# Optimization experiments

Measured on AMD Instinct MI355X. Metric: run time of the kernel, lower is better.

The kernel has to match this reference:

```python
import jax, jax.numpy as jnp
import numpy as np

T, H, I, E, K = 4096, 2048, 2048, 16, 4
EPS = 1e-6


def setup_inputs() -> dict:
    key = jax.random.key(0)
    ks = jax.random.split(key, 7)
    s = 0.02
    return {
        "x": jax.random.normal(ks[0], (T, H), dtype=jnp.float32),
        "gamma": jnp.ones((H,), dtype=jnp.float32),
        "wg": jax.random.normal(ks[1], (E, H), dtype=jnp.float32) * s,
        "bg": jax.random.normal(ks[2], (E,), dtype=jnp.float32) * s,
        "w1": jax.random.normal(ks[3], (E, I, H), dtype=jnp.float32) * s,  # gate proj
        "w3": jax.random.normal(ks[4], (E, I, H), dtype=jnp.float32) * s,  # up proj
        "w2": jax.random.normal(ks[5], (E, H, I), dtype=jnp.float32) * s,  # down proj
    }


def reference(x, gamma, wg, bg, w1, w3, w2):
    # RMSNorm
    t = x * jax.lax.rsqrt(jnp.mean(x * x, axis=-1, keepdims=True) + EPS) * gamma
    # Router: softmax -> top-k -> renormalize (FusedMoE renormalize=True)
    logits = t @ wg.T + bg                        # [T, E]
    probs = jax.nn.softmax(logits, axis=-1)
    vals, idx = jax.lax.top_k(probs, K)           # [T, K]
    vals = vals / jnp.sum(vals, axis=-1, keepdims=True)
    # Dense [T, E] routing-weight matrix (zeros outside top-k)
    route_w = jnp.einsum("tk,tke->te", vals, jax.nn.one_hot(idx, E, dtype=vals.dtype))
    # Grouped expert GEMMs: scan over experts, accumulate weighted outputs
    def body(acc, p):
        w1e, w3e, w2e, we = p                     # [I,H], [I,H], [H,I], [T]
        h = jax.nn.silu(t @ w1e.T) * (t @ w3e.T)  # [T, I]
        return acc + (h @ w2e.T) * we[:, None], None
    moe_out, _ = jax.lax.scan(body, jnp.zeros_like(x), (w1, w3, w2, route_w.T))
    return x + moe_out
```

## Files before the change

kernel.cpp:

```cpp
#include <hip/hip_runtime.h>
#include <hip/hip_bf16.h>

constexpr int TT = 4096;
constexpr int HH = 2048;
constexpr int II = 2048;
constexpr int EE = 16;
constexpr int KTOP = 4;

typedef __attribute__((ext_vector_type(4))) float f4;
typedef __attribute__((ext_vector_type(8))) short s8;

__device__ __forceinline__ short f2bf(float f) {
    union { __hip_bfloat16 b; short s; } u;
    u.b = __float2bfloat16(f);
    return u.s;
}
__device__ __forceinline__ float bf2f(short s) {
    union { unsigned u; float f; } v;
    v.u = ((unsigned)(unsigned short)s) << 16;
    return v.f;
}

__global__ void k_rmsnorm(const float* __restrict__ x, const float* __restrict__ gamma,
                          short* __restrict__ t16, int* __restrict__ cnt) {
    const int row = blockIdx.x;
    const int tid = threadIdx.x;
    if (row == 0 && tid < EE) cnt[tid] = 0;
    const f4* xr = (const f4*)(x + (size_t)row * HH);
    f4 v0 = xr[tid * 2], v1 = xr[tid * 2 + 1];
    float ss = 0.f;
#pragma unroll
    for (int i = 0; i < 4; i++) { ss += v0[i] * v0[i]; ss += v1[i] * v1[i]; }
#pragma unroll
    for (int m = 32; m >= 1; m >>= 1) ss += __shfl_xor(ss, m);
    __shared__ float red[4];
    const int wid = tid >> 6, lane = tid & 63;
    if (lane == 0) red[wid] = ss;
    __syncthreads();
    const float tot = red[0] + red[1] + red[2] + red[3];
    const float rs = rsqrtf(tot * (1.f / HH) + 1e-6f);
    const f4* gr = (const f4*)gamma;
    f4 g0 = gr[tid * 2], g1 = gr[tid * 2 + 1];
    s8 o;
#pragma unroll
    for (int i = 0; i < 4; i++) {
        o[i]     = f2bf(v0[i] * rs * g0[i]);
        o[4 + i] = f2bf(v1[i] * rs * g1[i]);
    }
    *(s8*)(t16 + (size_t)row * HH + tid * 8) = o;
}

__global__ void k_router(const float* __restrict__ x, const float* __restrict__ gamma,
                         const float* __restrict__ wg, const float* __restrict__ bg,
                         int* __restrict__ cnt, int* __restrict__ lst,
                         float* __restrict__ lwt) {
    const int lane = threadIdx.x & 63;
    const int tok = blockIdx.x * 4 + (threadIdx.x >> 6);
    const float* xr = x + (size_t)tok * HH;
    float t[32];
    float ss = 0.f;
#pragma unroll
    for (int j = 0; j < 32; j++) { float v = xr[lane + 64 * j]; t[j] = v; ss += v * v; }
#pragma unroll
    for (int m = 32; m >= 1; m >>= 1) ss += __shfl_xor(ss, m);
    const float rs = rsqrtf(ss * (1.f / HH) + 1e-6f);
#pragma unroll
    for (int j = 0; j < 32; j++) t[j] *= rs * gamma[lane + 64 * j];

    float logit[EE];
#pragma unroll
    for (int e = 0; e < EE; e++) {
        const float* wrow = wg + (size_t)e * HH;
        float a = 0.f;
#pragma unroll
        for (int j = 0; j < 32; j++) a += t[j] * wrow[lane + 64 * j];
#pragma unroll
        for (int m = 32; m >= 1; m >>= 1) a += __shfl_xor(a, m);
        logit[e] = a + bg[e];
    }
    unsigned chosen = 0u;
    int sel[KTOP]; float sv[KTOP];
#pragma unroll
    for (int k = 0; k < KTOP; k++) {
        float best = -1e30f; int bi = 0;
#pragma unroll
        for (int e = 0; e < EE; e++) {
            bool take = (!((chosen >> e) & 1u)) && (logit[e] > best);
            if (take) { best = logit[e]; bi = e; }
        }
        chosen |= 1u << bi; sel[k] = bi; sv[k] = best;
    }
    const float lmax = sv[0];
    float s = 0.f;
#pragma unroll
    for (int k = 0; k < KTOP; k++) { sv[k] = expf(sv[k] - lmax); s += sv[k]; }
    const float inv = 1.f / s;
    if (lane == 0) {
#pragma unroll
        for (int k = 0; k < KTOP; k++) {
            int e = sel[k];
            int p = atomicAdd(&cnt[e], 1);
            lst[e * TT + p] = tok * KTOP + k;
            lwt[e * TT + p] = sv[k] * inv;
        }
    }
}

__global__ __launch_bounds__(256, 2) void k_gemm_ffn_fused(
        const short* __restrict__ t16, const float* __restrict__ w1,
        const float* __restrict__ w3, short* __restrict__ h,
        const int* __restrict__ cnt, const int* __restrict__ lst) {
    const int e = blockIdx.z;
    const int Me = cnt[e];
    const int m0 = blockIdx.y * 128;
    if (m0 >= Me) return;
    const int n0 = blockIdx.x * 128;
    const float* we1 = w1 + (size_t)e * II * HH;
    const float* we3 = w3 + (size_t)e * II * HH;

    __shared__ char lA[16384];
    __shared__ char lB1[16384];
    __shared__ char lB2[16384];
    __shared__ int s_tok[128];

    const int tid = threadIdx.x;
    if (tid < 128) s_tok[tid] = (m0 + tid < Me) ? lst[e * TT + m0 + tid] : 0;
    __syncthreads();

    const int lane = tid & 63, wid = tid >> 6;
    const int wr = wid >> 1, wc = wid & 1;

    f4 acc1[4][4], acc2[4][4];
    const f4 zero = {0.f, 0.f, 0.f, 0.f};
#pragma unroll
    for (int i = 0; i < 4; i++)
#pragma unroll
        for (int j = 0; j < 4; j++) { acc1[i][j] = zero; acc2[i][j] = zero; }

    const int rbase = tid >> 3;
    const int kc = (tid & 7) * 8;
    const int lb0 = rbase * 128 + ((kc * 2) ^ ((rbase & 7) << 4));
    int tokrow[4];
#pragma unroll
    for (int j = 0; j < 4; j++) tokrow[j] = s_tok[rbase + 32 * j] >> 2;

    for (int kt = 0; kt < HH / 64; ++kt) {
        __syncthreads();
#pragma unroll
        for (int j = 0; j < 4; j++) {
            s8 av = *(const s8*)(t16 + (size_t)tokrow[j] * HH + kt * 64 + kc);
            *(s8*)(lA + lb0 + 4096 * j) = av;
        }
#pragma unroll
        for (int j = 0; j < 4; j++) {
            size_t roff = (size_t)(n0 + rbase + 32 * j) * HH + kt * 64 + kc;
            {
                f4 b0 = *(const f4*)(we1 + roff);
                f4 b1 = *(const f4*)(we1 + roff + 4);
                s8 bv;
#pragma unroll
                for (int i = 0; i < 4; i++) { bv[i] = f2bf(b0[i]); bv[4 + i] = f2bf(b1[i]); }
                *(s8*)(lB1 + lb0 + 4096 * j) = bv;
            }
            {
                f4 b0 = *(const f4*)(we3 + roff);
                f4 b1 = *(const f4*)(we3 + roff + 4);
                s8 bv;
#pragma unroll
                for (int i = 0; i < 4; i++) { bv[i] = f2bf(b0[i]); bv[4 + i] = f2bf(b1[i]); }
                *(s8*)(lB2 + lb0 + 4096 * j) = bv;
            }
        }
        __syncthreads();
#pragma unroll
        for (int kk = 0; kk < 2; ++kk) {
            s8 af[4], b1v[4], b2v[4];
#pragma unroll
            for (int mf = 0; mf < 4; mf++) {
                int r = wr * 64 + mf * 16 + (lane & 15);
                int byte = r * 128 + (((kk * 64) + ((lane >> 4) << 4)) ^ ((r & 7) << 4));
                af[mf] = *(const s8*)(lA + byte);
            }
#pragma unroll
            for (int nf = 0; nf < 4; nf++) {
                int r = wc * 64 + nf * 16 + (lane & 15);
                int byte = r * 128 + (((kk * 64) + ((lane >> 4) << 4)) ^ ((r & 7) << 4));
                b1v[nf] = *(const s8*)(lB1 + byte);
                b2v[nf] = *(const s8*)(lB2 + byte);
            }
#pragma unroll
            for (int mf = 0; mf < 4; mf++)
#pragma unroll
                for (int nf = 0; nf < 4; nf++) {
                    acc1[mf][nf] = __builtin_amdgcn_mfma_f32_16x16x32_bf16(
                        af[mf], b1v[nf], acc1[mf][nf], 0, 0, 0);
                    acc2[mf][nf] = __builtin_amdgcn_mfma_f32_16x16x32_bf16(
                        af[mf], b2v[nf], acc2[mf][nf], 0, 0, 0);
                }
        }
    }
#pragma unroll
    for (int mf = 0; mf < 4; mf++) {
#pragma unroll
        for (int j = 0; j < 4; j++) {
            int rl = wr * 64 + mf * 16 + ((lane >> 4) << 2) + j;
            if (m0 + rl < Me) {
                size_t orow = (size_t)s_tok[rl] * II;
#pragma unroll
                for (int nf = 0; nf < 4; nf++) {
                    int ncol = n0 + wc * 64 + nf * 16 + (lane & 15);
                    float g = acc1[mf][nf][j];
                    float u = acc2[mf][nf][j];
                    float sg = g / (1.f + expf(-g));
                    h[orow + ncol] = f2bf(sg * u);
                }
            }
        }
    }
}

__global__ __launch_bounds__(256) void k_gemm_down(
        const short* __restrict__ h, const float* __restrict__ w2,
        short* __restrict__ buf2, const int* __restrict__ cnt,
        const int* __restrict__ lst, const float* __restrict__ lwt) {
    const int e = blockIdx.z;
    const int Me = cnt[e];
    const int m0 = blockIdx.y * 128;
    if (m0 >= Me) return;
    const int n0 = blockIdx.x * 128;
    const float* we = w2 + (size_t)e * HH * II;

    __shared__ char lA[16384];
    __shared__ char lB[16384];
    __shared__ int s_tok[128];
    __shared__ float s_wgt[128];

    const int tid = threadIdx.x;
    if (tid < 128) {
        bool v = (m0 + tid < Me);
        s_tok[tid] = v ? lst[e * TT + m0 + tid] : 0;
        s_wgt[tid] = v ? lwt[e * TT + m0 + tid] : 0.f;
    }
    __syncthreads();

    const int lane = tid & 63, wid = tid >> 6;
    const int wr = wid >> 1, wc = wid & 1;

    f4 acc[4][4];
    const f4 zero = {0.f, 0.f, 0.f, 0.f};
#pragma unroll
    for (int i = 0; i < 4; i++)
#pragma unroll
        for (int j = 0; j < 4; j++) acc[i][j] = zero;

    const int rbase = tid >> 3;
    const int kc = (tid & 7) * 8;
    const int lb0 = rbase * 128 + ((kc * 2) ^ ((rbase & 7) << 4));
    int arow[4];
#pragma unroll
    for (int j = 0; j < 4; j++) arow[j] = s_tok[rbase + 32 * j];

    for (int kt = 0; kt < II / 64; ++kt) {
        __syncthreads();
#pragma unroll
        for (int j = 0; j < 4; j++) {
            s8 av = *(const s8*)(h + (size_t)arow[j] * II + kt * 64 + kc);
            *(s8*)(lA + lb0 + 4096 * j) = av;
        }
#pragma unroll
        for (int j = 0; j < 4; j++) {
            const float* gp = we + (size_t)(n0 + rbase + 32 * j) * II + kt * 64 + kc;
            f4 b0 = *(const f4*)gp;
            f4 b1 = *(const f4*)(gp + 4);
            s8 bv;
#pragma unroll
            for (int i = 0; i < 4; i++) { bv[i] = f2bf(b0[i]); bv[4 + i] = f2bf(b1[i]); }
            *(s8*)(lB + lb0 + 4096 * j) = bv;
        }
        __syncthreads();
#pragma unroll
        for (int kk = 0; kk < 2; ++kk) {
            s8 af[4], bfr[4];
#pragma unroll
            for (int mf = 0; mf < 4; mf++) {
                int r = wr * 64 + mf * 16 + (lane & 15);
                int byte = r * 128 + (((kk * 64) + ((lane >> 4) << 4)) ^ ((r & 7) << 4));
                af[mf] = *(const s8*)(lA + byte);
            }
#pragma unroll
            for (int nf = 0; nf < 4; nf++) {
                int r = wc * 64 + nf * 16 + (lane & 15);
                int byte = r * 128 + (((kk * 64) + ((lane >> 4) << 4)) ^ ((r & 7) << 4));
                bfr[nf] = *(const s8*)(lB + byte);
            }
#pragma unroll
            for (int mf = 0; mf < 4; mf++)
#pragma unroll
                for (int nf = 0; nf < 4; nf++)
                    acc[mf][nf] = __builtin_amdgcn_mfma_f32_16x16x32_bf16(
                        af[mf], bfr[nf], acc[mf][nf], 0, 0, 0);
        }
    }
#pragma unroll
    for (int mf = 0; mf < 4; mf++) {
#pragma unroll
        for (int j = 0; j < 4; j++) {
            int rl = wr * 64 + mf * 16 + ((lane >> 4) << 2) + j;
            if (m0 + rl < Me) {
                size_t orow = (size_t)s_tok[rl] * HH;
                float wgt = s_wgt[rl];
#pragma unroll
                for (int nf = 0; nf < 4; nf++) {
                    int ncol = n0 + wc * 64 + nf * 16 + (lane & 15);
                    buf2[orow + ncol] = f2bf(acc[mf][nf][j] * wgt);
                }
            }
        }
    }
}

__global__ void k_final(const float* __restrict__ x, const short* __restrict__ buf2,
                        float* __restrict__ out) {
    size_t i8 = (size_t)blockIdx.x * 256 + threadIdx.x;
    size_t tok = i8 / (HH / 8);
    size_t c8 = i8 % (HH / 8);
    const f4* xp = (const f4*)x + i8 * 2;
    f4 r0 = xp[0], r1 = xp[1];
#pragma unroll
    for (int k = 0; k < KTOP; k++) {
        s8 b = ((const s8*)buf2)[(tok * KTOP + k) * (HH / 8) + c8];
#pragma unroll
        for (int j = 0; j < 4; j++) { r0[j] += bf2f(b[j]); r1[j] += bf2f(b[4 + j]); }
    }
    ((f4*)out)[i8 * 2] = r0;
    ((f4*)out)[i8 * 2 + 1] = r1;
}

extern "C" void kernel_launch(void* const* d_in, const int* in_sizes, int n_in,
                              void* d_out, int out_size, void* d_ws, size_t ws_size,
                              hipStream_t stream) {
    const float* x     = (const float*)d_in[0];
    const float* gamma = (const float*)d_in[1];
    const float* wg    = (const float*)d_in[2];
    const float* bg    = (const float*)d_in[3];
    const float* w1    = (const float*)d_in[4];
    const float* w3    = (const float*)d_in[5];
    const float* w2    = (const float*)d_in[6];
    float* out = (float*)d_out;

    char* ws = (char*)d_ws;
    size_t off = 0;
    short* t16  = (short*)(ws + off); off += (size_t)TT * HH * 2;
    short* h1   = (short*)(ws + off); off += (size_t)TT * KTOP * II * 2;
    short* buf2 = (short*)(ws + off); off += (size_t)TT * KTOP * HH * 2;
    int* cnt    = (int*)(ws + off); off += 256;
    int* lst    = (int*)(ws + off); off += (size_t)EE * TT * 4;
    float* lwt  = (float*)(ws + off); off += (size_t)EE * TT * 4;

    k_rmsnorm<<<TT, 256, 0, stream>>>(x, gamma, t16, cnt);
    k_router<<<TT / 4, 256, 0, stream>>>(x, gamma, wg, bg, cnt, lst, lwt);

    dim3 g1(II / 128, TT / 128, EE);
    k_gemm_ffn_fused<<<g1, 256, 0, stream>>>(t16, w1, w3, h1, cnt, lst);

    dim3 g2(HH / 128, TT / 128, EE);
    k_gemm_down<<<g2, 256, 0, stream>>>(h1, w2, buf2, cnt, lst, lwt);

    k_final<<<(TT * HH / 8) / 256, 256, 0, stream>>>(x, buf2, out);
}
```

Measured before the change: 923.0 us.

## Register-prefetch next K tile in both expert GEMMs to overlap loads with MFMA

```diff
diff --git a/kernel.cpp b/kernel.cpp
--- a/kernel.cpp
+++ b/kernel.cpp
@@ -140,37 +140,43 @@
     const int rbase = tid >> 3;
     const int kc = (tid & 7) * 8;
     const int lb0 = rbase * 128 + ((kc * 2) ^ ((rbase & 7) << 4));
-    int tokrow[4];
-#pragma unroll
-    for (int j = 0; j < 4; j++) tokrow[j] = s_tok[rbase + 32 * j] >> 2;
-
-    for (int kt = 0; kt < HH / 64; ++kt) {
+    const short* gA[4]; const float* gB1[4]; const float* gB3[4];
+#pragma unroll
+    for (int j = 0; j < 4; j++) {
+        gA[j] = t16 + (size_t)(s_tok[rbase + 32 * j] >> 2) * HH + kc;
+        size_t roff = (size_t)(n0 + rbase + 32 * j) * HH + kc;
+        gB1[j] = we1 + roff;
+        gB3[j] = we3 + roff;
+    }
+
+    s8 ar[4]; f4 b1r[4][2]; f4 b3r[4][2];
+#define PREFETCH(kt)                                                           \
+    _Pragma("unroll")                                                          \
+    for (int j = 0; j < 4; j++) {                                              \
+        ar[j] = *(const s8*)(gA[j] + (kt) * 64);                               \
+        b1r[j][0] = *(const f4*)(gB1[j] + (kt) * 64);                          \
+        b1r[j][1] = *(const f4*)(gB1[j] + (kt) * 64 + 4);                      \
+        b3r[j][0] = *(const f4*)(gB3[j] + (kt) * 64);                          \
+        b3r[j][1] = *(const f4*)(gB3[j] + (kt) * 64 + 4);                      \
+    }
+
+    PREFETCH(0);
+    const int nkt = HH / 64;
+    for (int kt = 0; kt < nkt; ++kt) {
         __syncthreads();
 #pragma unroll
         for (int j = 0; j < 4; j++) {
-            s8 av = *(const s8*)(t16 + (size_t)tokrow[j] * HH + kt * 64 + kc);
-            *(s8*)(lA + lb0 + 4096 * j) = av;
-        }
-#pragma unroll
-        for (int j = 0; j < 4; j++) {
-            size_t roff = (size_t)(n0 + rbase + 32 * j) * HH + kt * 64 + kc;
-            {
-                f4 b0 = *(const f4*)(we1 + roff);
-                f4 b1 = *(const f4*)(we1 + roff + 4);
-                s8 bv;
-#pragma unroll
-                for (int i = 0; i < 4; i++) { bv[i] = f2bf(b0[i]); bv[4 + i] = f2bf(b1[i]); }
-                *(s8*)(lB1 + lb0 + 4096 * j) = bv;
-            }
-            {
-                f4 b0 = *(const f4*)(we3 + roff);
-                f4 b1 = *(const f4*)(we3 + roff + 4);
-                s8 bv;
-#pragma unroll
-                for (int i = 0; i < 4; i++) { bv[i] = f2bf(b0[i]); bv[4 + i] = f2bf(b1[i]); }
-                *(s8*)(lB2 + lb0 + 4096 * j) = bv;
-            }
-        }
+            *(s8*)(lA + lb0 + 4096 * j) = ar[j];
+            s8 bv1, bv3;
+#pragma unroll
+            for (int i = 0; i < 4; i++) {
+                bv1[i] = f2bf(b1r[j][0][i]); bv1[4 + i] = f2bf(b1r[j][1][i]);
+                bv3[i] = f2bf(b3r[j][0][i]); bv3[4 + i] = f2bf(b3r[j][1][i]);
+            }
+            *(s8*)(lB1 + lb0 + 4096 * j) = bv1;
+            *(s8*)(lB2 + lb0 + 4096 * j) = bv3;
+        }
+        if (kt + 1 < nkt) PREFETCH(kt + 1);
         __syncthreads();
 #pragma unroll
         for (int kk = 0; kk < 2; ++kk) {
@@ -199,6 +205,7 @@
                 }
         }
     }
+#undef PREFETCH
 #pragma unroll
     for (int mf = 0; mf < 4; mf++) {
 #pragma unroll
@@ -219,7 +226,7 @@
     }
 }
 
-__global__ __launch_bounds__(256) void k_gemm_down(
+__global__ __launch_bounds__(256, 2) void k_gemm_down(
         const short* __restrict__ h, const float* __restrict__ w2,
         short* __restrict__ buf2, const int* __restrict__ cnt,
         const int* __restrict__ lst, const float* __restrict__ lwt) {
@@ -256,27 +263,35 @@
     const int rbase = tid >> 3;
     const int kc = (tid & 7) * 8;
     const int lb0 = rbase * 128 + ((kc * 2) ^ ((rbase & 7) << 4));
-    int arow[4];
-#pragma unroll
-    for (int j = 0; j < 4; j++) arow[j] = s_tok[rbase + 32 * j];
-
-    for (int kt = 0; kt < II / 64; ++kt) {
+    const short* gA[4]; const float* gB[4];
+#pragma unroll
+    for (int j = 0; j < 4; j++) {
+        gA[j] = h + (size_t)s_tok[rbase + 32 * j] * II + kc;
+        gB[j] = we + (size_t)(n0 + rbase + 32 * j) * II + kc;
+    }
+
+    s8 ar[4]; f4 br[4][2];
+#define PREFETCH(kt)                                                           \
+    _Pragma("unroll")                                                          \
+    for (int j = 0; j < 4; j++) {                                              \
+        ar[j] = *(const s8*)(gA[j] + (kt) * 64);                               \
+        br[j][0] = *(const f4*)(gB[j] + (kt) * 64);                            \
+        br[j][1] = *(const f4*)(gB[j] + (kt) * 64 + 4);                        \
+    }
+
+    PREFETCH(0);
+    const int nkt = II / 64;
+    for (int kt = 0; kt < nkt; ++kt) {
         __syncthreads();
 #pragma unroll
         for (int j = 0; j < 4; j++) {
-            s8 av = *(const s8*)(h + (size_t)arow[j] * II + kt * 64 + kc);
-            *(s8*)(lA + lb0 + 4096 * j) = av;
-        }
-#pragma unroll
-        for (int j = 0; j < 4; j++) {
-            const float* gp = we + (size_t)(n0 + rbase + 32 * j) * II + kt * 64 + kc;
-            f4 b0 = *(const f4*)gp;
-            f4 b1 = *(const f4*)(gp + 4);
+            *(s8*)(lA + lb0 + 4096 * j) = ar[j];
             s8 bv;
 #pragma unroll
-            for (int i = 0; i < 4; i++) { bv[i] = f2bf(b0[i]); bv[4 + i] = f2bf(b1[i]); }
+            for (int i = 0; i < 4; i++) { bv[i] = f2bf(br[j][0][i]); bv[4 + i] = f2bf(br[j][1][i]); }
             *(s8*)(lB + lb0 + 4096 * j) = bv;
         }
+        if (kt + 1 < nkt) PREFETCH(kt + 1);
         __syncthreads();
 #pragma unroll
         for (int kk = 0; kk < 2; ++kk) {
@@ -301,6 +316,7 @@
                         af[mf], bfr[nf], acc[mf][nf], 0, 0, 0);
         }
     }
+#undef PREFETCH
 #pragma unroll
     for (int mf = 0; mf < 4; mf++) {
 #pragma unroll
```

New measurement: 1.199 ms. 1.3x slower.

## Fuse RMSNorm into router and register-prefetch next K tile in down GEMM

Applied to the files above, without the earlier changes.

```diff
diff --git a/kernel.cpp b/kernel.cpp
--- a/kernel.cpp
+++ b/kernel.cpp
@@ -21,39 +21,10 @@
     return v.f;
 }
 
-__global__ void k_rmsnorm(const float* __restrict__ x, const float* __restrict__ gamma,
-                          short* __restrict__ t16, int* __restrict__ cnt) {
-    const int row = blockIdx.x;
-    const int tid = threadIdx.x;
-    if (row == 0 && tid < EE) cnt[tid] = 0;
-    const f4* xr = (const f4*)(x + (size_t)row * HH);
-    f4 v0 = xr[tid * 2], v1 = xr[tid * 2 + 1];
-    float ss = 0.f;
-#pragma unroll
-    for (int i = 0; i < 4; i++) { ss += v0[i] * v0[i]; ss += v1[i] * v1[i]; }
-#pragma unroll
-    for (int m = 32; m >= 1; m >>= 1) ss += __shfl_xor(ss, m);
-    __shared__ float red[4];
-    const int wid = tid >> 6, lane = tid & 63;
-    if (lane == 0) red[wid] = ss;
-    __syncthreads();
-    const float tot = red[0] + red[1] + red[2] + red[3];
-    const float rs = rsqrtf(tot * (1.f / HH) + 1e-6f);
-    const f4* gr = (const f4*)gamma;
-    f4 g0 = gr[tid * 2], g1 = gr[tid * 2 + 1];
-    s8 o;
-#pragma unroll
-    for (int i = 0; i < 4; i++) {
-        o[i]     = f2bf(v0[i] * rs * g0[i]);
-        o[4 + i] = f2bf(v1[i] * rs * g1[i]);
-    }
-    *(s8*)(t16 + (size_t)row * HH + tid * 8) = o;
-}
-
 __global__ void k_router(const float* __restrict__ x, const float* __restrict__ gamma,
                          const float* __restrict__ wg, const float* __restrict__ bg,
-                         int* __restrict__ cnt, int* __restrict__ lst,
-                         float* __restrict__ lwt) {
+                         short* __restrict__ t16, int* __restrict__ cnt,
+                         int* __restrict__ lst, float* __restrict__ lwt) {
     const int lane = threadIdx.x & 63;
     const int tok = blockIdx.x * 4 + (threadIdx.x >> 6);
     const float* xr = x + (size_t)tok * HH;
@@ -66,6 +37,10 @@
     const float rs = rsqrtf(ss * (1.f / HH) + 1e-6f);
 #pragma unroll
     for (int j = 0; j < 32; j++) t[j] *= rs * gamma[lane + 64 * j];
+
+    short* tr = t16 + (size_t)tok * HH;
+#pragma unroll
+    for (int j = 0; j < 32; j++) tr[lane + 64 * j] = f2bf(t[j]);
 
     float logit[EE];
 #pragma unroll
@@ -219,7 +194,7 @@
     }
 }
 
-__global__ __launch_bounds__(256) void k_gemm_down(
+__global__ __launch_bounds__(256, 2) void k_gemm_down(
         const short* __restrict__ h, const float* __restrict__ w2,
         short* __restrict__ buf2, const int* __restrict__ cnt,
         const int* __restrict__ lst, const float* __restrict__ lwt) {
@@ -256,28 +231,40 @@
     const int rbase = tid >> 3;
     const int kc = (tid & 7) * 8;
     const int lb0 = rbase * 128 + ((kc * 2) ^ ((rbase & 7) << 4));
-    int arow[4];
-#pragma unroll
-    for (int j = 0; j < 4; j++) arow[j] = s_tok[rbase + 32 * j];
-
-    for (int kt = 0; kt < II / 64; ++kt) {
-        __syncthreads();
-#pragma unroll
-        for (int j = 0; j < 4; j++) {
-            s8 av = *(const s8*)(h + (size_t)arow[j] * II + kt * 64 + kc);
-            *(s8*)(lA + lb0 + 4096 * j) = av;
-        }
-#pragma unroll
-        for (int j = 0; j < 4; j++) {
-            const float* gp = we + (size_t)(n0 + rbase + 32 * j) * II + kt * 64 + kc;
-            f4 b0 = *(const f4*)gp;
-            f4 b1 = *(const f4*)(gp + 4);
+    const short* gA[4]; const float* gB[4];
+#pragma unroll
+    for (int j = 0; j < 4; j++) {
+        gA[j] = h + (size_t)s_tok[rbase + 32 * j] * II + kc;
+        gB[j] = we + (size_t)(n0 + rbase + 32 * j) * II + kc;
+    }
+
+    s8 ar[4]; f4 br[4][2];
+#define PREFETCH(kt)                                                           \
+    _Pragma("unroll")                                                          \
+    for (int j = 0; j < 4; j++) {                                              \
+        ar[j] = *(const s8*)(gA[j] + (kt) * 64);                               \
+        br[j][0] = *(const f4*)(gB[j] + (kt) * 64);                            \
+        br[j][1] = *(const f4*)(gB[j] + (kt) * 64 + 4);                        \
+    }
+
+    PREFETCH(0);
+    const int nkt = II / 64;
+    for (int kt = 0; kt < nkt; ++kt) {
+        asm volatile("" ::: "memory");
+        __builtin_amdgcn_s_barrier();
+        asm volatile("" ::: "memory");
+#pragma unroll
+        for (int j = 0; j < 4; j++) {
+            *(s8*)(lA + lb0 + 4096 * j) = ar[j];
             s8 bv;
 #pragma unroll
-            for (int i = 0; i < 4; i++) { bv[i] = f2bf(b0[i]); bv[4 + i] = f2bf(b1[i]); }
+            for (int i = 0; i < 4; i++) { bv[i] = f2bf(br[j][0][i]); bv[4 + i] = f2bf(br[j][1][i]); }
             *(s8*)(lB + lb0 + 4096 * j) = bv;
         }
-        __syncthreads();
+        if (kt + 1 < nkt) PREFETCH(kt + 1);
+        asm volatile("s_waitcnt lgkmcnt(0)" ::: "memory");
+        __builtin_amdgcn_s_barrier();
+        asm volatile("" ::: "memory");
 #pragma unroll
         for (int kk = 0; kk < 2; ++kk) {
             s8 af[4], bfr[4];
@@ -301,6 +288,7 @@
                         af[mf], bfr[nf], acc[mf][nf], 0, 0, 0);
         }
     }
+#undef PREFETCH
 #pragma unroll
     for (int mf = 0; mf < 4; mf++) {
 #pragma unroll
@@ -357,8 +345,8 @@
     int* lst    = (int*)(ws + off); off += (size_t)EE * TT * 4;
     float* lwt  = (float*)(ws + off); off += (size_t)EE * TT * 4;
 
-    k_rmsnorm<<<TT, 256, 0, stream>>>(x, gamma, t16, cnt);
-    k_router<<<TT / 4, 256, 0, stream>>>(x, gamma, wg, bg, cnt, lst, lwt);
+    hipMemsetAsync(cnt, 0, EE * sizeof(int), stream);
+    k_router<<<TT / 4, 256, 0, stream>>>(x, gamma, wg, bg, t16, cnt, lst, lwt);
 
     dim3 g1(II / 128, TT / 128, EE);
     k_gemm_ffn_fused<<<g1, 256, 0, stream>>>(t16, w1, w3, h1, cnt, lst);
```

Measured after the change: 912.4 us. No clear change (-1.1%).
